# Performance work log

Measured on AMD Instinct MI355X. Metric: run time of the kernel, lower is better.

Reference implementation:

```python
import jax, jax.numpy as jnp
import numpy as np

N_NODES = 50000
N_EDGES = 800000
D = 64  # node_dim == edge_dim
NEG_SLOPE = 0.2
EPS = 1e-5


def _lin_params(key, d_in, d_out):
    k1, k2 = jax.random.split(key)
    bound = 1.0 / np.sqrt(d_in)
    W = jax.random.uniform(k1, (d_out, d_in), minval=-bound, maxval=bound, dtype=jnp.float32)
    b = jax.random.uniform(k2, (d_out,), minval=-bound, maxval=bound, dtype=jnp.float32)
    return W, b


def setup_inputs() -> dict:
    key = jax.random.key(0)
    ks = jax.random.split(key, 12)
    V = jax.random.normal(ks[0], (N_NODES, D), dtype=jnp.float32)
    E = jax.random.normal(ks[1], (N_EDGES, D), dtype=jnp.float32)
    src = jax.random.randint(ks[2], (N_EDGES,), 0, N_NODES, dtype=jnp.int32)
    dst = jax.random.randint(ks[3], (N_EDGES,), 0, N_NODES, dtype=jnp.int32)
    pA_w, pA_b = _lin_params(ks[4], D, D)   # NodePooling.A
    pB_w, pB_b = _lin_params(ks[5], D, D)   # NodePooling.B
    mW1, mb1 = _lin_params(ks[6], D, D)     # edge MLP layer 1
    mW2, mb2 = _lin_params(ks[7], D, D)     # edge MLP layer 2
    BW, Bb = _lin_params(ks[8], D, D)       # GenMessage.B (scale)
    CW, Cb = _lin_params(ks[9], D, D)       # GenMessage.C (shift)
    return {"V": V, "E": E, "src": src, "dst": dst,
            "pA_w": pA_w, "pA_b": pA_b, "pB_w": pB_w, "pB_b": pB_b,
            "mW1": mW1, "mb1": mb1, "mW2": mW2, "mb2": mb2,
            "BW": BW, "Bb": Bb, "CW": CW, "Cb": Cb}


def _lrelu(x):
    return jnp.where(x >= 0, x, NEG_SLOPE * x)


def reference(V, E, src, dst, pA_w, pA_b, pB_w, pB_b, mW1, mb1, mW2, mb2, BW, Bb, CW, Cb):
    n = V.shape[0]
    # V = act(V); NodePooling: B(lrelu(A(V)))
    Va = _lrelu(V)
    Vp = _lrelu(Va @ pA_w.T + pA_b) @ pB_w.T + pB_b  # [N, D]
    # edge MLP on edge features (2 Linear+ReLU layers)
    x = jax.nn.relu(E @ mW1.T + mb1)
    x = jax.nn.relu(x @ mW2.T + mb2)                  # [E, D]
    scale = jax.nn.sigmoid(x @ BW.T + Bb)
    shift = x @ CW.T + Cb
    # gathered src features, gated affine message
    M1 = scale * Vp[src] + shift                      # [E, D]
    M2 = M1 * M1
    # segment-mean onto dst (DGL fn.mean); zero for isolated nodes
    deg = jax.ops.segment_sum(jnp.ones((dst.shape[0],), jnp.float32), dst, num_segments=n)
    denom = jnp.maximum(deg, 1.0)[:, None]
    V1 = jax.ops.segment_sum(M1, dst, num_segments=n) / denom
    V2 = jax.ops.segment_sum(M2, dst, num_segments=n) / denom
    return jnp.sqrt(jax.nn.relu(V2 - V1) + EPS)
```

## Files before the change

kernel.cpp:

```cpp
#include <hip/hip_runtime.h>

#define NN 50000
#define NE 800000
#define DDIM 64
#define PADX 68
#define PADS 68
#define NB_SCAN ((NN + 255) / 256)
#define NPB ((NN + 63) / 64)
#define NEG_SLOPE 0.2f
#define EPS_V 1e-5f

typedef short bf16x8 __attribute__((ext_vector_type(8)));
typedef float f32x4 __attribute__((ext_vector_type(4)));

__device__ __forceinline__ float lrelu_f(float x) { return x >= 0.0f ? x : NEG_SLOPE * x; }

__device__ __forceinline__ unsigned short bf16_rn(float x) {
    union { float f; unsigned int u; } c; c.f = x;
    unsigned int r = c.u + 0x7FFF + ((c.u >> 16) & 1);
    return (unsigned short)(r >> 16);
}
__device__ __forceinline__ float bf16_tof(unsigned short h) {
    union { float f; unsigned int u; } c; c.u = ((unsigned int)h) << 16;
    return c.f;
}

__device__ __forceinline__ unsigned cvtpk_bf16(float a, float b) {
    unsigned r;
    asm("v_cvt_pk_bf16_f32 %0, %1, %2" : "=v"(r) : "v"(a), "v"(b));
    return r;
}

__device__ __forceinline__ void split8(const float* __restrict__ v, bf16x8& h, bf16x8& l)
{
    union { bf16x8 v8; unsigned u[4]; } H, L;
    #pragma unroll
    for (int k = 0; k < 4; ++k) {
        float a = v[2*k], b = v[2*k+1];
        unsigned p = cvtpk_bf16(a, b);
        union { float f; unsigned u; } h0, h1;
        h0.u = p << 16;
        h1.u = p & 0xFFFF0000u;
        unsigned q = cvtpk_bf16(a - h0.f, b - h1.f);
        H.u[k] = p;
        L.u[k] = q;
    }
    h = H.v8; l = L.v8;
}

__device__ __forceinline__ void mma_tile(float acc[16], const float* __restrict__ XT,
                                         const float* __restrict__ Wc, int e0, int f0)
{
    #pragma unroll 4
    for (int kk = 0; kk < DDIM; kk += 4) {
        float4 A0 = *(const float4*)&XT[(kk+0)*PADX + e0];
        float4 A1 = *(const float4*)&XT[(kk+1)*PADX + e0];
        float4 A2 = *(const float4*)&XT[(kk+2)*PADX + e0];
        float4 A3 = *(const float4*)&XT[(kk+3)*PADX + e0];
        float4 B0 = *(const float4*)&Wc[(f0+0)*PADX + kk];
        float4 B1 = *(const float4*)&Wc[(f0+1)*PADX + kk];
        float4 B2 = *(const float4*)&Wc[(f0+2)*PADX + kk];
        float4 B3 = *(const float4*)&Wc[(f0+3)*PADX + kk];
        const float a[4][4] = {{A0.x,A0.y,A0.z,A0.w},{A1.x,A1.y,A1.z,A1.w},
                               {A2.x,A2.y,A2.z,A2.w},{A3.x,A3.y,A3.z,A3.w}};
        const float b[4][4] = {{B0.x,B0.y,B0.z,B0.w},{B1.x,B1.y,B1.z,B1.w},
                               {B2.x,B2.y,B2.z,B2.w},{B3.x,B3.y,B3.z,B3.w}};
        #pragma unroll
        for (int j = 0; j < 4; ++j)
            #pragma unroll
            for (int i = 0; i < 4; ++i)
                #pragma unroll
                for (int q = 0; q < 4; ++q)
                    acc[i*4+j] = fmaf(a[q][i], b[j][q], acc[i*4+j]);
    }
}

__device__ __forceinline__ void load_w_f32(float* __restrict__ Wc, const float* __restrict__ Wg, int tid)
{
    #pragma unroll
    for (int c = 0; c < 4; ++c) {
        int idx = (c << 10) + (tid << 2);
        int f = idx >> 6, k = idx & 63;
        *(float4*)&Wc[f*PADX + k] = *(const float4*)&Wg[idx];
    }
}

__global__ __launch_bounds__(256, 3)
void node_pool_kernel(const float* __restrict__ V,
                      const float* __restrict__ Aw, const float* __restrict__ Ab,
                      const float* __restrict__ Bw, const float* __restrict__ Bbv,
                      float* __restrict__ Vp,
                      const int* __restrict__ dst, int* __restrict__ degi,
                      const float* __restrict__ W1, const float* __restrict__ W2,
                      const float* __restrict__ WB, const float* __restrict__ WC,
                      short* __restrict__ WF)
{
    __shared__ float Wc[DDIM*PADX];
    __shared__ float XT[DDIM*PADX];
    const int tid = threadIdx.x;

    if (blockIdx.x >= NPB) {
        int gid = (blockIdx.x - NPB) * 256 + tid;
        int L = gid >> 12, r = gid & 4095;
        int t = r >> 10, ks = (r >> 9) & 1, lane = (r >> 3) & 63, j = r & 7;
        const float* Ws = (L == 0) ? W1 : (L == 1) ? W2 : (L == 2) ? WB : WC;
        int n = lane & 15, kg = lane >> 4;
        int f = t*16 + n, k = ks*32 + kg*8 + j;
        float v = Ws[f*64 + k];
        unsigned short h = bf16_rn(v);
        unsigned short l = bf16_rn(v - bf16_tof(h));
        int base = L*8192 + ((t*2 + ks)*2)*512 + lane*8 + j;
        WF[base]       = (short)h;
        WF[base + 512] = (short)l;

        const int stride = gridDim.x * 256;
        for (int e = blockIdx.x * 256 + tid; e < NE; e += stride)
            atomicAdd(&degi[dst[e]], 1);
        return;
    }

    const int nb = blockIdx.x * 64;
    const int e0 = (tid & 15) << 2;
    const int f0 = (tid >> 4) << 2;

    #pragma unroll
    for (int c = 0; c < 4; ++c) {
        int idx = (c << 10) + (tid << 2);
        int e = idx >> 6, d = idx & 63;
        int row = nb + e; if (row > NN-1) row = NN-1;
        float4 v = *(const float4*)&V[(size_t)row*DDIM + d];
        XT[(d+0)*PADX + e] = lrelu_f(v.x);
        XT[(d+1)*PADX + e] = lrelu_f(v.y);
        XT[(d+2)*PADX + e] = lrelu_f(v.z);
        XT[(d+3)*PADX + e] = lrelu_f(v.w);
    }
    load_w_f32(Wc, Aw, tid);
    __syncthreads();

    float acc[16];
    #pragma unroll
    for (int i = 0; i < 16; ++i) acc[i] = 0.f;
    mma_tile(acc, XT, Wc, e0, f0);
    __syncthreads();

    {
        float4 bv = *(const float4*)&Ab[f0];
        const float ba[4] = {bv.x, bv.y, bv.z, bv.w};
        #pragma unroll
        for (int j = 0; j < 4; ++j) {
            float4 v;
            v.x = lrelu_f(acc[0*4+j] + ba[j]);
            v.y = lrelu_f(acc[1*4+j] + ba[j]);
            v.z = lrelu_f(acc[2*4+j] + ba[j]);
            v.w = lrelu_f(acc[3*4+j] + ba[j]);
            *(float4*)&XT[(f0+j)*PADX + e0] = v;
        }
    }
    load_w_f32(Wc, Bw, tid);
    __syncthreads();

    float acc2[16];
    #pragma unroll
    for (int i = 0; i < 16; ++i) acc2[i] = 0.f;
    mma_tile(acc2, XT, Wc, e0, f0);

    float4 bv = *(const float4*)&Bbv[f0];
    #pragma unroll
    for (int i = 0; i < 4; ++i) {
        int row = nb + e0 + i;
        if (row < NN) {
            float4 o;
            o.x = acc2[i*4+0] + bv.x;
            o.y = acc2[i*4+1] + bv.y;
            o.z = acc2[i*4+2] + bv.z;
            o.w = acc2[i*4+3] + bv.w;
            *(float4*)&Vp[(size_t)row*DDIM + f0] = o;
        }
    }

    const int stride = gridDim.x * 256;
    for (int e = blockIdx.x * 256 + tid; e < NE; e += stride)
        atomicAdd(&degi[dst[e]], 1);
}

__global__ __launch_bounds__(256)
void scan1_kernel(const int* __restrict__ degi, int* __restrict__ linc, int* __restrict__ bsum)
{
    __shared__ int ws[4];
    const int tid = threadIdx.x;
    const int lane = tid & 63, wv = tid >> 6;
    int i = blockIdx.x * 256 + tid;
    int v = (i < NN) ? degi[i] : 0;
    int sc = v;
    #pragma unroll
    for (int off = 1; off < 64; off <<= 1) {
        int t = __shfl_up(sc, off, 64);
        if (lane >= off) sc += t;
    }
    if (lane == 63) ws[wv] = sc;
    __syncthreads();
    int wb = 0;
    #pragma unroll
    for (int w = 0; w < 4; ++w) if (w < wv) wb += ws[w];
    int incl = sc + wb;
    if (i < NN) linc[i] = incl;
    if (tid == 255) bsum[blockIdx.x] = incl;
}

__global__ __launch_bounds__(256)
void scan23_kernel(const int* __restrict__ degi, const int* __restrict__ linc,
                   const int* __restrict__ bsum, int* __restrict__ curs)
{
    __shared__ int ws[4];
    __shared__ int base_s;
    const int tid = threadIdx.x;
    const int lane = tid & 63, wv = tid >> 6;
    int v = (tid < NB_SCAN) ? bsum[tid] : 0;
    int sc = v;
    #pragma unroll
    for (int off = 1; off < 64; off <<= 1) {
        int t = __shfl_up(sc, off, 64);
        if (lane >= off) sc += t;
    }
    if (lane == 63) ws[wv] = sc;
    __syncthreads();
    int wb = 0;
    #pragma unroll
    for (int w = 0; w < 4; ++w) if (w < wv) wb += ws[w];
    if (tid == blockIdx.x) base_s = sc + wb - v;
    __syncthreads();
    int i = blockIdx.x * 256 + tid;
    if (i < NN) curs[i] = base_s + linc[i] - degi[i];
}

__global__ __launch_bounds__(256)
void scatter_kernel(const int* __restrict__ dst, int* __restrict__ cursor, int* __restrict__ eidx)
{
    int e = blockIdx.x * 256 + threadIdx.x;
    if (e < NE) {
        int p = atomicAdd(&cursor[dst[e]], 1);
        eidx[p] = e;
    }
}

__device__ __forceinline__ void gemm64_dual_lds(const short* bw, int lane,
                                                const bf16x8 ah0[2], const bf16x8 al0[2],
                                                const bf16x8 ah1[2], const bf16x8 al1[2],
                                                f32x4 acc0[4], f32x4 acc1[4])
{
    #pragma unroll
    for (int ks = 0; ks < 2; ++ks) {
        bf16x8 bh[4], bl[4];
        #pragma unroll
        for (int t = 0; t < 4; ++t) {
            bh[t] = *(const bf16x8*)&bw[(((t*2 + ks)*2 + 0)*64 + lane)*8];
            bl[t] = *(const bf16x8*)&bw[(((t*2 + ks)*2 + 1)*64 + lane)*8];
        }
        #pragma unroll
        for (int t = 0; t < 4; ++t) {
            acc0[t] = __builtin_amdgcn_mfma_f32_16x16x32_bf16(al0[ks], bh[t], acc0[t], 0, 0, 0);
            acc1[t] = __builtin_amdgcn_mfma_f32_16x16x32_bf16(al1[ks], bh[t], acc1[t], 0, 0, 0);
            acc0[t] = __builtin_amdgcn_mfma_f32_16x16x32_bf16(ah0[ks], bl[t], acc0[t], 0, 0, 0);
            acc1[t] = __builtin_amdgcn_mfma_f32_16x16x32_bf16(ah1[ks], bl[t], acc1[t], 0, 0, 0);
            acc0[t] = __builtin_amdgcn_mfma_f32_16x16x32_bf16(ah0[ks], bh[t], acc0[t], 0, 0, 0);
            acc1[t] = __builtin_amdgcn_mfma_f32_16x16x32_bf16(ah1[ks], bh[t], acc1[t], 0, 0, 0);
        }
    }
}

__device__ __forceinline__ void transpose_frags(float* __restrict__ sw, const f32x4 y[4],
                                                int lane, bf16x8 ah[2], bf16x8 al[2])
{
    const int n = lane & 15, mg = lane >> 4;
    #pragma unroll
    for (int t = 0; t < 4; ++t)
        #pragma unroll
        for (int r = 0; r < 4; ++r)
            sw[(mg*4 + r)*PADS + t*16 + n] = y[t][r];
    __builtin_amdgcn_wave_barrier();
    const int m = lane & 15, kg = lane >> 4;
    float x[16];
    *(float4*)&x[0]  = *(const float4*)&sw[m*PADS + kg*8];
    *(float4*)&x[4]  = *(const float4*)&sw[m*PADS + kg*8 + 4];
    *(float4*)&x[8]  = *(const float4*)&sw[m*PADS + 32 + kg*8];
    *(float4*)&x[12] = *(const float4*)&sw[m*PADS + 32 + kg*8 + 4];
    split8(&x[0], ah[0], al[0]);
    split8(&x[8], ah[1], al[1]);
    __builtin_amdgcn_wave_barrier();
}

__global__ __launch_bounds__(256, 3)
void edge_fused_kernel(const float* __restrict__ Eg,
                       const int* __restrict__ src, const int* __restrict__ dst,
                       const int* __restrict__ eidx,
                       const short* __restrict__ WF,
                       const float* __restrict__ b1, const float* __restrict__ b2,
                       const float* __restrict__ bB, const float* __restrict__ bC,
                       const float* __restrict__ Vp,
                       float* __restrict__ S1, float* __restrict__ S2)
{
    __shared__ __align__(16) short bw[8192];
    __shared__ float scratch[4 * 16 * PADS];
    __shared__ int aux[4 * 64];

    const int tid = threadIdx.x;
    const int lane = tid & 63, wv = tid >> 6;
    float* sw = scratch + wv * 16 * PADS;
    int* auxw = aux + wv * 64;

    const int ew = blockIdx.x * 128 + wv * 32;
    const int m = lane & 15, kg = lane >> 4;
    const int n = lane & 15, mg = lane >> 4;

    uint4 w0, w1, w2, w3;
    #define ISSUE_W(Wg) do { const uint4* s_ = (const uint4*)(Wg); \
        w0 = s_[tid]; w1 = s_[256 + tid]; w2 = s_[512 + tid]; w3 = s_[768 + tid]; } while (0)
    #define COMMIT_W() do { __syncthreads(); uint4* d_ = (uint4*)bw; \
        d_[tid] = w0; d_[256 + tid] = w1; d_[512 + tid] = w2; d_[768 + tid] = w3; \
        __syncthreads(); } while (0)

    ISSUE_W(WF);

    if (lane < 32) {
        int eg = eidx[ew + lane];
        auxw[lane]      = src[eg];
        auxw[32 + lane] = dst[eg];
    }
    bf16x8 ah0[2], al0[2], ah1[2], al1[2];
    {
        int eg0 = eidx[ew + m];
        int eg1 = eidx[ew + 16 + m];
        const float* er0 = Eg + (size_t)eg0*DDIM + kg*8;
        const float* er1 = Eg + (size_t)eg1*DDIM + kg*8;
        float x[16];
        *(float4*)&x[0]  = *(const float4*)&er0[0];
        *(float4*)&x[4]  = *(const float4*)&er0[4];
        *(float4*)&x[8]  = *(const float4*)&er0[32];
        *(float4*)&x[12] = *(const float4*)&er0[36];
        split8(&x[0], ah0[0], al0[0]);
        split8(&x[8], ah0[1], al0[1]);
        *(float4*)&x[0]  = *(const float4*)&er1[0];
        *(float4*)&x[4]  = *(const float4*)&er1[4];
        *(float4*)&x[8]  = *(const float4*)&er1[32];
        *(float4*)&x[12] = *(const float4*)&er1[36];
        split8(&x[0], ah1[0], al1[0]);
        split8(&x[8], ah1[1], al1[1]);
    }

    COMMIT_W();
    ISSUE_W(WF + 8192);
    f32x4 acc0[4], acc1[4];
    #pragma unroll
    for (int t = 0; t < 4; ++t) { acc0[t] = (f32x4){0.f,0.f,0.f,0.f}; acc1[t] = (f32x4){0.f,0.f,0.f,0.f}; }
    __builtin_amdgcn_s_setprio(1);
    gemm64_dual_lds(bw, lane, ah0, al0, ah1, al1, acc0, acc1);
    __builtin_amdgcn_s_setprio(0);
    #pragma unroll
    for (int t = 0; t < 4; ++t) {
        float b = b1[t*16 + n];
        #pragma unroll
        for (int r = 0; r < 4; ++r) {
            acc0[t][r] = fmaxf(acc0[t][r] + b, 0.0f);
            acc1[t][r] = fmaxf(acc1[t][r] + b, 0.0f);
        }
    }
    transpose_frags(sw, acc0, lane, ah0, al0);
    transpose_frags(sw, acc1, lane, ah1, al1);

    COMMIT_W();
    ISSUE_W(WF + 2*8192);
    #pragma unroll
    for (int t = 0; t < 4; ++t) { acc0[t] = (f32x4){0.f,0.f,0.f,0.f}; acc1[t] = (f32x4){0.f,0.f,0.f,0.f}; }
    __builtin_amdgcn_s_setprio(1);
    gemm64_dual_lds(bw, lane, ah0, al0, ah1, al1, acc0, acc1);
    __builtin_amdgcn_s_setprio(0);
    #pragma unroll
    for (int t = 0; t < 4; ++t) {
        float b = b2[t*16 + n];
        #pragma unroll
        for (int r = 0; r < 4; ++r) {
            acc0[t][r] = fmaxf(acc0[t][r] + b, 0.0f);
            acc1[t][r] = fmaxf(acc1[t][r] + b, 0.0f);
        }
    }
    transpose_frags(sw, acc0, lane, ah0, al0);
    transpose_frags(sw, acc1, lane, ah1, al1);

    COMMIT_W();
    ISSUE_W(WF + 3*8192);
    f32x4 accS0[4], accS1[4];
    #pragma unroll
    for (int t = 0; t < 4; ++t) { accS0[t] = (f32x4){0.f,0.f,0.f,0.f}; accS1[t] = (f32x4){0.f,0.f,0.f,0.f}; }
    __builtin_amdgcn_s_setprio(1);
    gemm64_dual_lds(bw, lane, ah0, al0, ah1, al1, accS0, accS1);
    __builtin_amdgcn_s_setprio(0);

    COMMIT_W();
    f32x4 accH0[4], accH1[4];
    #pragma unroll
    for (int t = 0; t < 4; ++t) { accH0[t] = (f32x4){0.f,0.f,0.f,0.f}; accH1[t] = (f32x4){0.f,0.f,0.f,0.f}; }
    __builtin_amdgcn_s_setprio(1);
    gemm64_dual_lds(bw, lane, ah0, al0, ah1, al1, accH0, accH1);
    __builtin_amdgcn_s_setprio(0);

    const int f = lane;
    float s1 = 0.f, s2 = 0.f;
    int prev = auxw[32];
    #pragma unroll
    for (int tile = 0; tile < 2; ++tile) {
        const int to = tile * 16;
        f32x4* accS = tile ? accS1 : accS0;
        f32x4* accH = tile ? accH1 : accH0;

        {
            int sn[4];
            #pragma unroll
            for (int r = 0; r < 4; ++r) sn[r] = auxw[to + mg*4 + r];
            #pragma unroll
            for (int t = 0; t < 4; ++t) {
                const int ff = t*16 + n;
                const float bBv = bB[ff];
                const float bCv = bC[ff];
                #pragma unroll
                for (int r = 0; r < 4; ++r) {
                    float vp = Vp[(size_t)sn[r]*DDIM + ff];
                    float sg = 1.0f / (1.0f + __expf(-(accS[t][r] + bBv)));
                    sw[(mg*4 + r)*PADS + ff] = fmaf(sg, vp, accH[t][r] + bCv);
                }
            }
        }
        __builtin_amdgcn_wave_barrier();

        #pragma unroll 4
        for (int e = 0; e < 16; ++e) {
            int dn = auxw[32 + to + e];
            float m1 = sw[e*PADS + f];
            float m2 = m1 * m1;
            if (dn != prev) {
                atomicAdd(&S1[(size_t)prev*DDIM + f], s1);
                atomicAdd(&S2[(size_t)prev*DDIM + f], s2);
                s1 = 0.f; s2 = 0.f; prev = dn;
            }
            s1 += m1; s2 += m2;
        }
        __builtin_amdgcn_wave_barrier();
    }
    atomicAdd(&S1[(size_t)prev*DDIM + f], s1);
    atomicAdd(&S2[(size_t)prev*DDIM + f], s2);
    #undef ISSUE_W
    #undef COMMIT_W
}

__global__ __launch_bounds__(256)
void finalize_kernel(const float* __restrict__ S1, const float* __restrict__ S2,
                     const int* __restrict__ degi, float* __restrict__ out)
{
    int gid = blockIdx.x * blockDim.x + threadIdx.x;
    if (gid >= NN*DDIM) return;
    int n = gid >> 6;
    float dn = (float)degi[n];
    dn = dn > 1.0f ? dn : 1.0f;
    float v = (S2[gid] - S1[gid]) / dn;
    out[gid] = sqrtf(fmaxf(v, 0.0f) + EPS_V);
}

extern "C" void kernel_launch(void* const* d_in, const int* in_sizes, int n_in,
                              void* d_out, int out_size, void* d_ws, size_t ws_size,
                              hipStream_t stream) {
    const float* V   = (const float*)d_in[0];
    const float* Eg  = (const float*)d_in[1];
    const int*   src = (const int*)d_in[2];
    const int*   dst = (const int*)d_in[3];
    const float* pAw = (const float*)d_in[4];
    const float* pAb = (const float*)d_in[5];
    const float* pBw = (const float*)d_in[6];
    const float* pBb = (const float*)d_in[7];
    const float* mW1 = (const float*)d_in[8];
    const float* mb1 = (const float*)d_in[9];
    const float* mW2 = (const float*)d_in[10];
    const float* mb2 = (const float*)d_in[11];
    const float* BW  = (const float*)d_in[12];
    const float* Bb  = (const float*)d_in[13];
    const float* CW  = (const float*)d_in[14];
    const float* Cb  = (const float*)d_in[15];
    float* out = (float*)d_out;

    float* ws    = (float*)d_ws;
    float* Vp    = ws;
    float* S1    = ws + (size_t)NN*DDIM;
    float* S2    = ws + (size_t)2*NN*DDIM;
    int*   degi  = (int*)(ws + (size_t)3*NN*DDIM);
    int*   curs  = degi + NN;
    int*   linc  = curs + NN;
    int*   bsum  = linc + NN;
    int*   eidx  = bsum + NB_SCAN;
    short* WF    = (short*)(eidx + NE);

    hipMemsetAsync(S1, 0, (size_t)(2*NN*DDIM + NN) * sizeof(float), stream);

    node_pool_kernel<<<NPB + 64, 256, 0, stream>>>(V, pAw, pAb, pBw, pBb, Vp, dst, degi,
                                                   mW1, mW2, BW, CW, WF);
    scan1_kernel<<<NB_SCAN, 256, 0, stream>>>(degi, linc, bsum);
    scan23_kernel<<<NB_SCAN, 256, 0, stream>>>(degi, linc, bsum, curs);
    scatter_kernel<<<(NE + 255)/256, 256, 0, stream>>>(dst, curs, eidx);
    edge_fused_kernel<<<NE/128, 256, 0, stream>>>(Eg, src, dst, eidx, WF,
                                                  mb1, mb2, Bb, Cb, Vp, S1, S2);
    finalize_kernel<<<(NN*DDIM + 255)/256, 256, 0, stream>>>(S1, S2, degi, out);
}
```

Measured before the change: 491.3 us.

## Fuse scan, offset and scatter kernels into one grid-synchronized CSR build kernel

Merges the two scan kernels and the edge-scatter kernel into a single persistent kernel of 196 blocks that uses global atomic spin barriers between phases. The zeroing of the S1/S2 accumulators also moves out of the hipMemsetAsync and into this kernel, so the memset now clears only the small integer region. The aim is to remove two kernel launches and a large memset. In exchange, the scatter phase runs on only 196 blocks instead of 3125, and the spin barriers assume every block is resident at the same time.

```diff
diff --git a/kernel.cpp b/kernel.cpp
--- a/kernel.cpp
+++ b/kernel.cpp
@@ -184,61 +184,83 @@
 }
 
 __global__ __launch_bounds__(256)
-void scan1_kernel(const int* __restrict__ degi, int* __restrict__ linc, int* __restrict__ bsum)
-{
-    __shared__ int ws[4];
-    const int tid = threadIdx.x;
-    const int lane = tid & 63, wv = tid >> 6;
-    int i = blockIdx.x * 256 + tid;
-    int v = (i < NN) ? degi[i] : 0;
-    int sc = v;
-    #pragma unroll
-    for (int off = 1; off < 64; off <<= 1) {
-        int t = __shfl_up(sc, off, 64);
-        if (lane >= off) sc += t;
-    }
-    if (lane == 63) ws[wv] = sc;
-    __syncthreads();
-    int wb = 0;
-    #pragma unroll
-    for (int w = 0; w < 4; ++w) if (w < wv) wb += ws[w];
-    int incl = sc + wb;
-    if (i < NN) linc[i] = incl;
-    if (tid == 255) bsum[blockIdx.x] = incl;
-}
-
-__global__ __launch_bounds__(256)
-void scan23_kernel(const int* __restrict__ degi, const int* __restrict__ linc,
-                   const int* __restrict__ bsum, int* __restrict__ curs)
+void csr_build_kernel(const int* __restrict__ degi, int* __restrict__ linc,
+                      int* __restrict__ bsum, int* __restrict__ curs,
+                      const int* __restrict__ dst, int* __restrict__ eidx,
+                      float* __restrict__ Szero,
+                      int* __restrict__ bar)
 {
     __shared__ int ws[4];
     __shared__ int base_s;
     const int tid = threadIdx.x;
     const int lane = tid & 63, wv = tid >> 6;
-    int v = (tid < NB_SCAN) ? bsum[tid] : 0;
-    int sc = v;
-    #pragma unroll
-    for (int off = 1; off < 64; off <<= 1) {
-        int t = __shfl_up(sc, off, 64);
-        if (lane >= off) sc += t;
-    }
-    if (lane == 63) ws[wv] = sc;
-    __syncthreads();
-    int wb = 0;
-    #pragma unroll
-    for (int w = 0; w < 4; ++w) if (w < wv) wb += ws[w];
-    if (tid == blockIdx.x) base_s = sc + wb - v;
-    __syncthreads();
-    int i = blockIdx.x * 256 + tid;
-    if (i < NN) curs[i] = base_s + linc[i] - degi[i];
-}
-
-__global__ __launch_bounds__(256)
-void scatter_kernel(const int* __restrict__ dst, int* __restrict__ cursor, int* __restrict__ eidx)
-{
-    int e = blockIdx.x * 256 + threadIdx.x;
-    if (e < NE) {
-        int p = atomicAdd(&cursor[dst[e]], 1);
+    const int gstride = NB_SCAN * 256;
+
+    {
+        float4 z = {0.f, 0.f, 0.f, 0.f};
+        float4* p = (float4*)Szero;
+        const int total = 2 * NN * DDIM / 4;
+        for (int i = blockIdx.x * 256 + tid; i < total; i += gstride)
+            p[i] = z;
+    }
+
+    const int i = blockIdx.x * 256 + tid;
+    const int dv = (i < NN) ? degi[i] : 0;
+    {
+        int sc = dv;
+        #pragma unroll
+        for (int off = 1; off < 64; off <<= 1) {
+            int t = __shfl_up(sc, off, 64);
+            if (lane >= off) sc += t;
+        }
+        if (lane == 63) ws[wv] = sc;
+        __syncthreads();
+        int wb = 0;
+        #pragma unroll
+        for (int w = 0; w < 4; ++w) if (w < wv) wb += ws[w];
+        int incl = sc + wb;
+        if (i < NN) linc[i] = incl;
+        if (tid == 255) atomicExch(&bsum[blockIdx.x], incl);
+    }
+
+    __syncthreads();
+    if (tid == 0) {
+        __threadfence();
+        atomicAdd(&bar[0], 1);
+        while (atomicAdd(&bar[0], 0) < NB_SCAN) ;
+        __threadfence();
+    }
+    __syncthreads();
+
+    {
+        int v2 = (tid < NB_SCAN) ? atomicAdd(&bsum[tid], 0) : 0;
+        int sc2 = v2;
+        #pragma unroll
+        for (int off = 1; off < 64; off <<= 1) {
+            int t = __shfl_up(sc2, off, 64);
+            if (lane >= off) sc2 += t;
+        }
+        if (lane == 63) ws[wv] = sc2;
+        __syncthreads();
+        int wb2 = 0;
+        #pragma unroll
+        for (int w = 0; w < 4; ++w) if (w < wv) wb2 += ws[w];
+        if (tid == blockIdx.x) base_s = sc2 + wb2 - v2;
+        __syncthreads();
+        if (i < NN) atomicExch(&curs[i], base_s + linc[i] - dv);
+    }
+
+    __syncthreads();
+    if (tid == 0) {
+        __threadfence();
+        atomicAdd(&bar[1], 1);
+        while (atomicAdd(&bar[1], 0) < NB_SCAN) ;
+        __threadfence();
+    }
+    __syncthreads();
+
+    for (int e = blockIdx.x * 256 + tid; e < NE; e += gstride) {
+        int p = atomicAdd(&curs[dst[e]], 1);
         eidx[p] = e;
     }
 }
@@ -493,16 +515,16 @@
     int*   curs  = degi + NN;
     int*   linc  = curs + NN;
     int*   bsum  = linc + NN;
-    int*   eidx  = bsum + NB_SCAN;
+    int*   bar   = bsum + NB_SCAN;
+    int*   eidx  = bar + 2;
     short* WF    = (short*)(eidx + NE);
 
-    hipMemsetAsync(S1, 0, (size_t)(2*NN*DDIM + NN) * sizeof(float), stream);
+    hipMemsetAsync(degi, 0, (size_t)(3*NN + NB_SCAN + 2) * sizeof(int), stream);
 
     node_pool_kernel<<<NPB + 64, 256, 0, stream>>>(V, pAw, pAb, pBw, pBb, Vp, dst, degi,
                                                    mW1, mW2, BW, CW, WF);
-    scan1_kernel<<<NB_SCAN, 256, 0, stream>>>(degi, linc, bsum);
-    scan23_kernel<<<NB_SCAN, 256, 0, stream>>>(degi, linc, bsum, curs);
-    scatter_kernel<<<(NE + 255)/256, 256, 0, stream>>>(dst, curs, eidx);
+    csr_build_kernel<<<NB_SCAN, 256, 0, stream>>>(degi, linc, bsum, curs, dst, eidx,
+                                                  S1, bar);
     edge_fused_kernel<<<NE/128, 256, 0, stream>>>(Eg, src, dst, eidx, WF,
                                                   mb1, mb2, Bb, Cb, Vp, S1, S2);
     finalize_kernel<<<(NN*DDIM + 255)/256, 256, 0, stream>>>(S1, S2, degi, out);
```

Measured after the change: 504.5 us. +2.7%, slower.
